# Performance work log

Measured on AMD Instinct MI355X. Metric: run time of the kernel, lower is better.

## Reference

```python
import jax, jax.numpy as jnp
import numpy as np
from fractions import Fraction
from math import factorial

# ---------- e3nn-convention real Wigner 3j (computed once in numpy) ----------

def _su2_cg(j1, m1, j2, m2, j3, m3):
    if m3 != m1 + m2:
        return 0.0
    vmin = int(max(-j1 + j2 + m3, -j1 + m1, 0))
    vmax = int(min(j2 + j3 + m1, j3 - j1 + j2, j3 + m3))
    f = lambda n: factorial(round(n))
    C = ((2.0 * j3 + 1.0) * Fraction(
        f(j3 + j1 - j2) * f(j3 - j1 + j2) * f(j1 + j2 - j3) * f(j3 + m3) * f(j3 - m3),
        f(j1 + j2 + j3 + 1) * f(j1 - m1) * f(j1 + m1) * f(j2 - m2) * f(j2 + m2))) ** 0.5
    S = 0
    for v in range(vmin, vmax + 1):
        S += (-1) ** int(v + j2 + m2) * Fraction(
            f(j2 + j3 + m1 - v) * f(j1 - m1 + v),
            f(v) * f(j3 - j1 + j2 - v) * f(j3 + m3 - v) * f(v + j1 - j2 - m3))
    return float(C * S)

def _q_real2complex(l):
    q = np.zeros((2 * l + 1, 2 * l + 1), dtype=complex)
    for m in range(-l, 0):
        q[l + m, l + abs(m)] = 1 / 2 ** 0.5
        q[l + m, l - abs(m)] = -1j / 2 ** 0.5
    q[l, l] = 1.0
    for m in range(1, l + 1):
        q[l + m, l + abs(m)] = (-1) ** m / 2 ** 0.5
        q[l + m, l - abs(m)] = 1j * (-1) ** m / 2 ** 0.5
    return (-1j) ** l * q

def _w3j(l1, l2, l3):
    C = np.zeros((2 * l1 + 1, 2 * l2 + 1, 2 * l3 + 1), dtype=complex)
    for m1 in range(-l1, l1 + 1):
        for m2 in range(-l2, l2 + 1):
            for m3 in range(-l3, l3 + 1):
                C[l1 + m1, l2 + m2, l3 + m3] = _su2_cg(l1, m1, l2, m2, l3, m3)
    C = np.einsum('ij,kl,mn,ikn->jlm', _q_real2complex(l1), _q_real2complex(l2),
                  np.conj(_q_real2complex(l3).T), C)
    assert np.abs(C.imag).max() < 1e-7
    C = C.real
    return C / np.linalg.norm(C)

# uuw instructions from get_feasible_tp(hidden, hidden, 0e+1e+2e): (l1, l2, l_out)
INS = [(0, 0, 0), (0, 2, 2), (1, 1, 0), (1, 1, 1), (1, 1, 2), (2, 0, 2), (2, 2, 0), (2, 2, 1), (2, 2, 2)]
W3J = {ls: jnp.asarray(_w3j(*ls), dtype=jnp.float32) for ls in set(INS)}
# change of basis of ReducedTensorProducts('ij', i='1o'): sph(0e+1e+2e) -> cart 3x3
Q_COB = jnp.asarray(np.concatenate([(2 * l + 1) ** 0.5 * _w3j(1, 1, l).transpose(2, 0, 1)
                                    for l in (0, 1, 2)], axis=0), dtype=jnp.float32)  # (9,3,3)
IN_IRR = ((128, 0), (64, 1), (32, 2))  # edge_irreps, dim 480
HID = 16                               # hidden multiplicity per l
CART = jnp.array([2, 0, 1])            # e3nn (y,z,x) -> (x,y,z)

def _split(x):
    parts, o = [], 0
    for mul, l in IN_IRR:
        d = mul * (2 * l + 1)
        parts.append(x[:, o:o + d].reshape(-1, mul, 2 * l + 1))
        o += d
    return parts

def _lin(parts, Ws):  # e3nn o3.Linear: per-l channel mix, 1/sqrt(fan_in)
    return [jnp.einsum('nui,uv->nvi', p, W) * (1.0 / np.sqrt(p.shape[1])) for p, W in zip(parts, Ws)]

def _forward(batch, x_scalar, x_spherical, WU0, WU1, WU2, WV0, WV1, WV2,
             Wg1, bg1, Wg2, bg2, Wp0, Wp1, Wp2, num_graphs):
    xs = _split(x_spherical)
    hU = _lin(xs, (WU0, WU1, WU2))  # [(N,16,1),(N,16,3),(N,16,5)]
    hV = _lin(xs, (WV0, WV1, WV2))
    w = jax.nn.silu(x_scalar @ Wg1 + bg1) @ Wg2 + bg2  # (N, 144) per-path tp weights
    outs = {0: [], 1: [], 2: []}
    for k, (l1, l2, l3) in enumerate(INS):
        wk = w[:, k * HID:(k + 1) * HID]
        coeff = float(np.sqrt((2 * l3 + 1) / HID))  # component/element norm
        outs[l3].append(coeff * jnp.einsum('nu,ijm,nui,nuj->nm', wk, W3J[(l1, l2, l3)], hU[l1], hV[l2]))
    Wp = {0: Wp0, 1: Wp1, 2: Wp2}
    sph = [jnp.einsum('num,u->nm', jnp.stack(outs[l], 1), Wp[l][:, 0]) * (1.0 / np.sqrt(len(outs[l])))
           for l in (0, 1, 2)]  # lin_out_post -> 1x0e+1x1e+1x2e
    atom_out = jnp.concatenate(sph, axis=-1)  # (N, 9)
    res_sph = jax.ops.segment_sum(atom_out, batch, num_segments=num_graphs)  # (G, 9)
    res_cart = jnp.einsum('gk,kij->gij', res_sph, Q_COB)  # (G, 3, 3)
    return res_cart[:, CART][:, :, CART]

def setup_inputs():
    key = jax.random.key(0)
    k = jax.random.split(key, 16)
    N, G = 150000, 2000
    f32 = jnp.float32
    rn = lambda kk, shp, s=1.0: jax.random.normal(kk, shp, f32) * s
    return {
        'batch': jnp.sort(jax.random.randint(k[0], (N,), 0, G)),
        'x_scalar': rn(k[1], (N, 128)),
        'x_spherical': rn(k[2], (N, 480)),
        'WU0': rn(k[3], (128, 16)), 'WU1': rn(k[4], (64, 16)), 'WU2': rn(k[5], (32, 16)),
        'WV0': rn(k[6], (128, 16)), 'WV1': rn(k[7], (64, 16)), 'WV2': rn(k[8], (32, 16)),
        'Wg1': rn(k[9], (128, 64), 128 ** -0.5), 'bg1': jnp.zeros((64,), f32),
        'Wg2': rn(k[10], (64, 144), 64 ** -0.5), 'bg2': jnp.zeros((144,), f32),
        'Wp0': rn(k[11], (3, 1)), 'Wp1': rn(k[12], (2, 1)), 'Wp2': rn(k[13], (4, 1)),
        'num_graphs': G,
    }

def reference(batch, x_scalar, x_spherical, WU0, WU1, WU2, WV0, WV1, WV2,
              Wg1, bg1, Wg2, bg2, Wp0, Wp1, Wp2, num_graphs):
    return _forward(batch, x_scalar, x_spherical, WU0, WU1, WU2, WV0, WV1, WV2,
                    Wg1, bg1, Wg2, bg2, Wp0, Wp1, Wp2, num_graphs)
```

## Files before the change

### kernel.cpp

```cpp
#include <hip/hip_runtime.h>
#include <hip/hip_bf16.h>
#include <math.h>

typedef unsigned short u16;
typedef unsigned int   u32;

#define TILE 16

#define WS_FLAG  368
#define WS_WG1   384
#define WS_WG2   8576
#define WS_WU0   17792
#define WS_WU1   19840
#define WS_WU2   20864
#define WS_WV0   21376
#define WS_WV1   23424
#define WS_WV2   24448
#define WS_BG1   24960
#define WS_BG2   25024
#define WS_C9    25168
#define WS_RES   25216

__device__ __forceinline__ float b2f(u16 u){
  return __uint_as_float(((u32)u) << 16);
}
__device__ __forceinline__ float ldconv(const void* p, int i, int isbf){
  return isbf ? b2f(((const u16*)p)[i]) : ((const float*)p)[i];
}

__global__ void detect_kernel(const u32* __restrict__ words, int* __restrict__ flag){
  int t = threadIdx.x;
  int cnt = 0;
  for (int i = 0; i < 16; i++){
    u32 w = words[t*16 + i];
    u32 e = (w >> 7) & 0xFF;
    cnt += (e >= 117 && e <= 137) ? 1 : 0;
  }
  #pragma unroll
  for (int m = 1; m < 64; m <<= 1) cnt += __shfl_xor(cnt, m, 64);
  if (t == 0) *flag = (cnt > 512) ? 1 : 0;
}

__device__ double factd(int n){ double r=1.0; for(int i=2;i<=n;++i) r*=(double)i; return r; }

__device__ double su2_cg(int j1,int m1,int j2,int m2,int j3,int m3){
  if (m1+m2 != m3) return 0.0;
  int vmin = max(max(-j1+j2+m3, -j1+m1), 0);
  int vmax = min(min(j2+j3+m1, j3-j1+j2), j3+m3);
  double C = sqrt((2.0*j3+1.0)
      * factd(j3+j1-j2)*factd(j3-j1+j2)*factd(j1+j2-j3)*factd(j3+m3)*factd(j3-m3)
      / (factd(j1+j2+j3+1)*factd(j1-m1)*factd(j1+m1)*factd(j2-m2)*factd(j2+m2)));
  double S = 0.0;
  for (int v=vmin; v<=vmax; ++v){
    double t = factd(j2+j3+m1-v)*factd(j1-m1+v)
             / (factd(v)*factd(j3-j1+j2-v)*factd(j3+m3-v)*factd(v+j1-j2-m3));
    S += ((v+j2+m2)&1) ? -t : t;
  }
  return C*S;
}

__device__ void qmat_lds(int l, double* qre, double* qim){
  int d = 2*l+1;
  for (int i=0;i<d*d;i++){ qre[i]=0.0; qim[i]=0.0; }
  double s = 1.0/sqrt(2.0);
  for (int m=-l; m<0; ++m){
    qre[(l+m)*d + (l-m)] = s;
    qim[(l+m)*d + (l+m)] = -s;
  }
  qre[l*d + l] = 1.0;
  for (int m=1; m<=l; ++m){
    double sgn = (m&1) ? -1.0 : 1.0;
    qre[(l+m)*d + (l+m)] = sgn*s;
    qim[(l+m)*d + (l-m)] = sgn*s;
  }
  double fr, fi;
  switch (l & 3){ case 0: fr=1; fi=0; break; case 1: fr=0; fi=-1; break;
                  case 2: fr=-1; fi=0; break; default: fr=0; fi=1; }
  for (int i=0;i<d*d;i++){
    double a=qre[i], b=qim[i];
    qre[i]=a*fr-b*fi; qim[i]=a*fi+b*fr;
  }
}

__global__ void setup_kernel(float* __restrict__ ws){
  __shared__ double q1r[25], q1i[25], q2r[25], q2i[25], q3r[25], q3i[25];
  __shared__ double red[128];
  const int L1[9]={0,0,1,1,1,2,2,2,2};
  const int L2[9]={0,2,1,1,1,0,2,2,2};
  const int L3[9]={0,2,0,1,2,2,0,1,2};
  const int OFF[9]={0,1,26,35,62,107,132,157,232};
  const int b = blockIdx.x;
  const int l1=L1[b], l2=L2[b], l3=L3[b];
  const int d1=2*l1+1, d2=2*l2+1, d3=2*l3+1;
  const int tot = d1*d2*d3;
  const int t = threadIdx.x;

  if (t==0) qmat_lds(l1, q1r, q1i);
  if (t==1) qmat_lds(l2, q2r, q2i);
  if (t==2) qmat_lds(l3, q3r, q3i);
  __syncthreads();

  double ar = 0.0;
  if (t < tot){
    const int j = t/(d2*d3), rem = t - j*(d2*d3), l = rem/d3, m = rem - l*d3;
    for (int i=0;i<d1;i++){
      double a1r=q1r[i*d1+j], a1i=q1i[i*d1+j];
      for (int k=0;k<d2;k++){
        double a2r=q2r[k*d2+l], a2i=q2i[k*d2+l];
        double t12r = a1r*a2r - a1i*a2i;
        double t12i = a1r*a2i + a1i*a2r;
        for (int n=0;n<d3;n++){
          double c = su2_cg(l1, i-l1, l2, k-l2, l3, n-l3);
          if (c==0.0) continue;
          double a3r = q3r[n*d3+m], a3i = -q3i[n*d3+m];
          ar += c*(t12r*a3r - t12i*a3i);
        }
      }
    }
  }
  red[t] = ar*ar;
  __syncthreads();
  for (int s=64; s>0; s>>=1){
    if (t < s) red[t] += red[t+s];
    __syncthreads();
  }
  double nrm = sqrt(red[0]);
  if (t < tot) ws[OFF[b] + t] = (float)(ar/nrm);
}

__global__ void convert_weights(
    const void* Wg1, const void* Wg2,
    const void* WU0, const void* WU1, const void* WU2,
    const void* WV0, const void* WV1, const void* WV2,
    const void* bg1, const void* bg2,
    const void* Wp0, const void* Wp1, const void* Wp2,
    float* __restrict__ ws)
{
  const int isbf = ((const int*)ws)[WS_FLAG];
  const int b = blockIdx.x, t = threadIdx.x;
  if (b < 10){
    const void* src[10] = {Wg1,Wg2,WU0,WU1,WU2,WV0,WV1,WV2,bg1,bg2};
    const int   sz[10]  = {8192,9216,2048,1024,512,2048,1024,512,64,144};
    const int   off[10] = {WS_WG1,WS_WG2,WS_WU0,WS_WU1,WS_WU2,WS_WV0,WS_WV1,WS_WV2,WS_BG1,WS_BG2};
    const void* s = src[b]; float* d = ws + off[b]; int n = sz[b];
    for (int i = t; i < n; i += 256) d[i] = ldconv(s, i, isbf);
  } else if (b == 10 && t == 0){
    float* C9 = ws + WS_C9;
    const int l3k[9]  = {0,2,0,1,2,2,0,1,2};
    const int idxk[9] = {0,0,1,0,1,2,2,1,3};
    for (int k=0;k<9;k++){
      int l3 = l3k[k];
      const void* wp = (l3==0) ? Wp0 : (l3==1) ? Wp1 : Wp2;
      float wpv = ldconv(wp, idxk[k], isbf);
      float len = (l3==0) ? 3.f : (l3==1) ? 2.f : 4.f;
      C9[k] = sqrtf((2.f*l3 + 1.f)/16.f) * wpv * rsqrtf(len);
    }
  }
}

__device__ __forceinline__ void load8_bf16(const u16* p, float* dst){
  uint4 v = *reinterpret_cast<const uint4*>(p);
  u32 w[4] = {v.x, v.y, v.z, v.w};
  #pragma unroll
  for (int q=0;q<4;q++){
    dst[2*q]   = __uint_as_float((w[q] & 0xffffu) << 16);
    dst[2*q+1] = __uint_as_float(w[q] & 0xffff0000u);
  }
}
__device__ __forceinline__ void load8_f32(const float* p, float* dst){
  float4 v0 = *reinterpret_cast<const float4*>(p);
  float4 v1 = *reinterpret_cast<const float4*>(p+4);
  dst[0]=v0.x; dst[1]=v0.y; dst[2]=v0.z; dst[3]=v0.w;
  dst[4]=v1.x; dst[5]=v1.y; dst[6]=v1.z; dst[7]=v1.w;
}

__global__ __launch_bounds__(256) void main_kernel(
    const int* __restrict__ batch,
    const void* __restrict__ xscv,
    const void* __restrict__ xspv,
    const float* __restrict__ ws,
    float* __restrict__ res,
    int N)
{
  __shared__ float s_xsph[TILE][481];
  __shared__ float s_w[TILE][144];
  __shared__ float s_uni[4624];
  __shared__ float s_w3j[357];
  __shared__ float s_bg1[64];
  __shared__ float s_bg2[144];
  __shared__ float s_C[9];
  __shared__ int   s_batch[TILE];

  float (*s_xs)[128] = reinterpret_cast<float(*)[128]>(s_uni);
  float (*s_h1)[64]  = reinterpret_cast<float(*)[64]>(s_uni + 2048);
  float (*s_hU)[144] = reinterpret_cast<float(*)[144]>(s_uni);
  float (*s_hV)[144] = reinterpret_cast<float(*)[144]>(s_uni + 2304);

  const int tid  = threadIdx.x;
  const int wave = tid >> 6;
  const int lane = tid & 63;
  const int n0   = blockIdx.x * TILE;
  const int isbf = ((const int*)ws)[WS_FLAG];

  const float* wsWg1 = ws + WS_WG1;
  const float* wsWg2 = ws + WS_WG2;
  const float* wsWU0 = ws + WS_WU0;
  const float* wsWU1 = ws + WS_WU1;
  const float* wsWU2 = ws + WS_WU2;
  const float* wsWV0 = ws + WS_WV0;
  const float* wsWV1 = ws + WS_WV1;
  const float* wsWV2 = ws + WS_WV2;

  if (tid < TILE){ int n = n0 + tid; s_batch[tid] = (n < N) ? batch[n] : -1; }
  if (tid < 64)  s_bg1[tid] = ws[WS_BG1 + tid];
  if (tid < 144) s_bg2[tid] = ws[WS_BG2 + tid];
  if (tid < 9)   s_C[tid]   = ws[WS_C9 + tid];
  for (int i = tid; i < 357; i += 256) s_w3j[i] = ws[i];
  {
    int base = tid*8, row = base >> 7, col = base & 127;
    int n = n0 + row;
    if (n < N){
      if (isbf) load8_bf16((const u16*)xscv + (size_t)n*128 + col, &s_xs[row][col]);
      else      load8_f32 ((const float*)xscv + (size_t)n*128 + col, &s_xs[row][col]);
    } else { for (int q=0;q<8;q++) s_xs[row][col+q] = 0.f; }
  }
  {
    for (int it = tid; it < 960; it += 256){
      int base = it*8, row = base/480, col = base - row*480;
      int n = n0 + row;
      if (n < N){
        if (isbf) load8_bf16((const u16*)xspv + (size_t)n*480 + col, &s_xsph[row][col]);
        else      load8_f32 ((const float*)xspv + (size_t)n*480 + col, &s_xsph[row][col]);
      } else { for (int q=0;q<8;q++) s_xsph[row][col+q] = 0.f; }
    }
  }
  __syncthreads();

  {
    const int a0 = wave*4;
    float acc0=s_bg1[lane], acc1=acc0, acc2=acc0, acc3=acc0;
    for (int c=0;c<128;c++){
      float wv = wsWg1[c*64 + lane];
      acc0 += s_xs[a0+0][c]*wv;
      acc1 += s_xs[a0+1][c]*wv;
      acc2 += s_xs[a0+2][c]*wv;
      acc3 += s_xs[a0+3][c]*wv;
    }
    s_h1[a0+0][lane] = acc0/(1.f+__expf(-acc0));
    s_h1[a0+1][lane] = acc1/(1.f+__expf(-acc1));
    s_h1[a0+2][lane] = acc2/(1.f+__expf(-acc2));
    s_h1[a0+3][lane] = acc3/(1.f+__expf(-acc3));
  }
  __syncthreads();

  {
    const int a0 = wave*4;
    float acc[4][3];
    #pragma unroll
    for (int t=0;t<4;t++){
      acc[t][0] = s_bg2[lane];
      acc[t][1] = s_bg2[64+lane];
      acc[t][2] = (lane<16) ? s_bg2[128+lane] : 0.f;
    }
    for (int c=0;c<64;c++){
      float w0 = wsWg2[c*144 + lane];
      float w1 = wsWg2[c*144 + 64 + lane];
      float w2 = (lane<16) ? wsWg2[c*144 + 128 + lane] : 0.f;
      #pragma unroll
      for (int t=0;t<4;t++){
        float h = s_h1[a0+t][c];
        acc[t][0] += h*w0; acc[t][1] += h*w1; acc[t][2] += h*w2;
      }
    }
    #pragma unroll
    for (int t=0;t<4;t++){
      s_w[a0+t][lane]    = acc[t][0];
      s_w[a0+t][64+lane] = acc[t][1];
      if (lane < 16) s_w[a0+t][128+lane] = acc[t][2];
    }
  }
  __syncthreads();

  {
    const int a = tid >> 4, v = tid & 15;
    const float r128 = 0.088388347648318447f;
    const float r64  = 0.125f;
    const float r32  = 0.17677669529663689f;
    {
      float aU=0.f, aV=0.f;
      for (int u=0;u<128;u++){
        float x = s_xsph[a][u];
        aU += x*wsWU0[u*16+v];
        aV += x*wsWV0[u*16+v];
      }
      s_hU[a][v] = aU*r128; s_hV[a][v] = aV*r128;
    }
    {
      float aU[3]={0,0,0}, aV[3]={0,0,0};
      for (int u=0;u<64;u++){
        float wu = wsWU1[u*16+v], wv = wsWV1[u*16+v];
        #pragma unroll
        for (int i=0;i<3;i++){
          float x = s_xsph[a][128 + u*3 + i];
          aU[i] += x*wu; aV[i] += x*wv;
        }
      }
      #pragma unroll
      for (int i=0;i<3;i++){ s_hU[a][16+v*3+i]=aU[i]*r64; s_hV[a][16+v*3+i]=aV[i]*r64; }
    }
    {
      float aU[5]={0,0,0,0,0}, aV[5]={0,0,0,0,0};
      for (int u=0;u<32;u++){
        float wu = wsWU2[u*16+v], wv = wsWV2[u*16+v];
        #pragma unroll
        for (int i=0;i<5;i++){
          float x = s_xsph[a][320 + u*5 + i];
          aU[i] += x*wu; aV[i] += x*wv;
        }
      }
      #pragma unroll
      for (int i=0;i<5;i++){ s_hU[a][64+v*5+i]=aU[i]*r32; s_hV[a][64+v*5+i]=aV[i]*r32; }
    }
  }
  __syncthreads();

  {
    const int a = tid >> 4, u = tid & 15;
    float hu0 = s_hU[a][u], hv0 = s_hV[a][u];
    float hu1[3], hv1[3], hu2[5], hv2[5];
    #pragma unroll
    for (int i=0;i<3;i++){ hu1[i]=s_hU[a][16+u*3+i]; hv1[i]=s_hV[a][16+u*3+i]; }
    #pragma unroll
    for (int i=0;i<5;i++){ hu2[i]=s_hU[a][64+u*5+i]; hv2[i]=s_hV[a][64+u*5+i]; }
    float wk[9];
    #pragma unroll
    for (int k=0;k<9;k++) wk[k] = s_w[a][k*16+u];

    const float* J = s_w3j;
    float t9[9] = {0,0,0,0,0,0,0,0,0};

    t9[0] += s_C[0]*wk[0]*J[0]*hu0*hv0;
    {
      float cw = s_C[1]*wk[1]*hu0;
      #pragma unroll
      for (int m=0;m<5;m++){
        float s=0.f;
        #pragma unroll
        for (int j=0;j<5;j++) s += J[1 + j*5 + m]*hv2[j];
        t9[4+m] += cw*s;
      }
    }
    {
      float s=0.f;
      #pragma unroll
      for (int i=0;i<3;i++)
        #pragma unroll
        for (int j=0;j<3;j++) s += J[26 + i*3 + j]*hu1[i]*hv1[j];
      t9[0] += s_C[2]*wk[2]*s;
    }
    {
      float sm[3]={0,0,0};
      #pragma unroll
      for (int i=0;i<3;i++)
        #pragma unroll
        for (int j=0;j<3;j++){
          float p = hu1[i]*hv1[j];
          #pragma unroll
          for (int m=0;m<3;m++) sm[m] += J[35 + (i*3+j)*3 + m]*p;
        }
      float c = s_C[3]*wk[3];
      #pragma unroll
      for (int m=0;m<3;m++) t9[1+m] += c*sm[m];
    }
    {
      float sm[5]={0,0,0,0,0};
      #pragma unroll
      for (int i=0;i<3;i++)
        #pragma unroll
        for (int j=0;j<3;j++){
          float p = hu1[i]*hv1[j];
          #pragma unroll
          for (int m=0;m<5;m++) sm[m] += J[62 + (i*3+j)*5 + m]*p;
        }
      float c = s_C[4]*wk[4];
      #pragma unroll
      for (int m=0;m<5;m++) t9[4+m] += c*sm[m];
    }
    {
      float cw = s_C[5]*wk[5]*hv0;
      #pragma unroll
      for (int m=0;m<5;m++){
        float s=0.f;
        #pragma unroll
        for (int i=0;i<5;i++) s += J[107 + i*5 + m]*hu2[i];
        t9[4+m] += cw*s;
      }
    }
    {
      float s=0.f;
      #pragma unroll
      for (int i=0;i<5;i++)
        #pragma unroll
        for (int j=0;j<5;j++) s += J[132 + i*5 + j]*hu2[i]*hv2[j];
      t9[0] += s_C[6]*wk[6]*s;
    }
    {
      float sm[3]={0,0,0};
      #pragma unroll
      for (int i=0;i<5;i++)
        #pragma unroll
        for (int j=0;j<5;j++){
          float p = hu2[i]*hv2[j];
          #pragma unroll
          for (int m=0;m<3;m++) sm[m] += J[157 + (i*5+j)*3 + m]*p;
        }
      float c = s_C[7]*wk[7];
      #pragma unroll
      for (int m=0;m<3;m++) t9[1+m] += c*sm[m];
    }
    {
      float sm[5]={0,0,0,0,0};
      #pragma unroll
      for (int i=0;i<5;i++)
        #pragma unroll
        for (int j=0;j<5;j++){
          float p = hu2[i]*hv2[j];
          #pragma unroll
          for (int m=0;m<5;m++) sm[m] += J[232 + (i*5+j)*5 + m]*p;
        }
      float c = s_C[8]*wk[8];
      #pragma unroll
      for (int m=0;m<5;m++) t9[4+m] += c*sm[m];
    }

    #pragma unroll
    for (int mask=1; mask<16; mask<<=1){
      #pragma unroll
      for (int s=0;s<9;s++) t9[s] += __shfl_xor(t9[s], mask, 64);
    }
    if (u == 0 && (n0 + a) < N){
      int g = s_batch[a];
      float* r = res + (size_t)g*9;
      #pragma unroll
      for (int s=0;s<9;s++) atomicAdd(&r[s], t9[s]);
    }
  }
}

__global__ void finish_kernel(const float* __restrict__ res,
                              const float* __restrict__ ws,
                              void* __restrict__ out, int G)
{
  int idx = blockIdx.x*256 + threadIdx.x;
  if (idx >= G*9) return;
  const int isbf = ((const int*)ws)[WS_FLAG];
  int g = idx/9, s = idx - g*9;
  int a = s/3, b = s - a*3;
  const int cart[3] = {2,0,1};
  int ca = cart[a], cb = cart[b];
  const float s3 = 1.7320508075688772f, s5 = 2.2360679774997896f;
  const float* r = res + (size_t)g*9;
  float acc = r[0]*ws[26 + ca*3 + cb];
  #pragma unroll
  for (int m=0;m<3;m++) acc += r[1+m]*s3*ws[35 + (ca*3+cb)*3 + m];
  #pragma unroll
  for (int m=0;m<5;m++) acc += r[4+m]*s5*ws[62 + (ca*3+cb)*5 + m];
  if (isbf) ((__hip_bfloat16*)out)[idx] = __float2bfloat16(acc);
  else      ((float*)out)[idx] = acc;
}

extern "C" void kernel_launch(void* const* d_in, const int* in_sizes, int n_in,
                              void* d_out, int out_size, void* d_ws, size_t ws_size,
                              hipStream_t stream) {
  const int* batch = (const int*)d_in[0];
  const void* xsc = d_in[1];
  const void* xsp = d_in[2];

  const int N = in_sizes[0];
  const int G = out_size / 9;

  float* ws  = (float*)d_ws;
  float* res = ws + WS_RES;

  hipMemsetAsync(res, 0, (size_t)G*9*sizeof(float), stream);
  detect_kernel<<<1, 64, 0, stream>>>((const u32*)xsp, (int*)(ws + WS_FLAG));
  setup_kernel<<<9, 128, 0, stream>>>(ws);
  convert_weights<<<11, 256, 0, stream>>>(d_in[9], d_in[11],
                                          d_in[3], d_in[4], d_in[5],
                                          d_in[6], d_in[7], d_in[8],
                                          d_in[10], d_in[12],
                                          d_in[13], d_in[14], d_in[15],
                                          ws);

  int nb = (N + TILE - 1) / TILE;
  main_kernel<<<nb, 256, 0, stream>>>(batch, xsc, xsp, ws, res, N);

  finish_kernel<<<(G*9 + 255)/256, 256, 0, stream>>>(res, ws, d_out, G);
}
```

Before: 1.184 ms.

## Add bf16 MFMA path for gate MLP and projections with per-wave tiles

Adds an mfma_kernel that does the gate MLP and the U/V projections with 16x16x32 bf16 MFMA instructions. It uses pre-transposed bf16 weight copies in the workspace, with block-diagonal expansion for the l=1 and l=2 projections. Each wave handles one 16-atom tile and reduces per-graph results with shuffles and atomics. A probe kernel checks that the MFMA operand layout is correct, and the old fp32 kernel now exits early when the MFMA path applies. Splitting the hidden activations into hi and lo bf16 parts keeps precision, at the cost of extra MFMAs and redundant zero-padded work in the expanded weights.

Result: no change. 1.162 ms (-1.9%).

```diff
diff --git a/kernel.cpp b/kernel.cpp
--- a/kernel.cpp
+++ b/kernel.cpp
@@ -4,10 +4,13 @@
 
 typedef unsigned short u16;
 typedef unsigned int   u32;
+typedef __attribute__((ext_vector_type(8))) short short8v;
+typedef __attribute__((ext_vector_type(4))) float f32x4;
 
 #define TILE 16
 
 #define WS_FLAG  368
+#define WS_MOK   369
 #define WS_WG1   384
 #define WS_WG2   8576
 #define WS_WU0   17792
@@ -21,8 +24,19 @@
 #define WS_C9    25168
 #define WS_RES   25216
 
+#define WSH_BG1T 88064
+#define WSH_BG2T 96256
+#define WSH_B0T  105472
+#define WSH_B1T  109568
+#define WSH_B2T  128000
+#define WS_NEED_BYTES 307200
+
 __device__ __forceinline__ float b2f(u16 u){
   return __uint_as_float(((u32)u) << 16);
+}
+__device__ __forceinline__ u16 f2b(float f){
+  u32 x = __float_as_uint(f);
+  return (u16)((x + 0x7fffu + ((x >> 16) & 1u)) >> 16);
 }
 __device__ __forceinline__ float ldconv(const void* p, int i, int isbf){
   return isbf ? b2f(((const u16*)p)[i]) : ((const float*)p)[i];
@@ -138,29 +152,385 @@
 {
   const int isbf = ((const int*)ws)[WS_FLAG];
   const int b = blockIdx.x, t = threadIdx.x;
+  u16* wh = (u16*)ws;
   if (b < 10){
     const void* src[10] = {Wg1,Wg2,WU0,WU1,WU2,WV0,WV1,WV2,bg1,bg2};
     const int   sz[10]  = {8192,9216,2048,1024,512,2048,1024,512,64,144};
     const int   off[10] = {WS_WG1,WS_WG2,WS_WU0,WS_WU1,WS_WU2,WS_WV0,WS_WV1,WS_WV2,WS_BG1,WS_BG2};
     const void* s = src[b]; float* d = ws + off[b]; int n = sz[b];
     for (int i = t; i < n; i += 256) d[i] = ldconv(s, i, isbf);
-  } else if (b == 10 && t == 0){
-    float* C9 = ws + WS_C9;
-    const int l3k[9]  = {0,2,0,1,2,2,0,1,2};
-    const int idxk[9] = {0,0,1,0,1,2,2,1,3};
-    for (int k=0;k<9;k++){
-      int l3 = l3k[k];
-      const void* wp = (l3==0) ? Wp0 : (l3==1) ? Wp1 : Wp2;
-      float wpv = ldconv(wp, idxk[k], isbf);
-      float len = (l3==0) ? 3.f : (l3==1) ? 2.f : 4.f;
-      C9[k] = sqrtf((2.f*l3 + 1.f)/16.f) * wpv * rsqrtf(len);
-    }
+  } else if (b == 10){
+    if (t == 0){
+      float* C9 = ws + WS_C9;
+      const int l3k[9]  = {0,2,0,1,2,2,0,1,2};
+      const int idxk[9] = {0,0,1,0,1,2,2,1,3};
+      for (int k=0;k<9;k++){
+        int l3 = l3k[k];
+        const void* wp = (l3==0) ? Wp0 : (l3==1) ? Wp1 : Wp2;
+        float wpv = ldconv(wp, idxk[k], isbf);
+        float len = (l3==0) ? 3.f : (l3==1) ? 2.f : 4.f;
+        C9[k] = sqrtf((2.f*l3 + 1.f)/16.f) * wpv * rsqrtf(len);
+      }
+    }
+  } else if (b == 11){
+    for (int i=t;i<8192;i+=256){
+      int n = i >> 7, k = i & 127;
+      wh[WSH_BG1T + i] = f2b(ldconv(Wg1, k*64 + n, isbf));
+    }
+  } else if (b == 12){
+    for (int i=t;i<9216;i+=256){
+      int n = i >> 6, k = i & 63;
+      wh[WSH_BG2T + i] = f2b(ldconv(Wg2, k*144 + n, isbf));
+    }
+  } else if (b == 13){
+    for (int i=t;i<4096;i+=256){
+      int n = i >> 7, k = i & 127;
+      float v = (n < 16) ? ldconv(WU0, k*16 + n, isbf)
+                         : ldconv(WV0, k*16 + (n-16), isbf);
+      wh[WSH_B0T + i] = f2b(v);
+    }
+  } else if (b == 14){
+    for (int i=t;i<18432;i+=256){
+      int n = i / 192, k = i - n*192;
+      int uv = n / 48, rem = n - uv*48, ii = rem >> 4, vv = rem & 15;
+      float val = 0.f;
+      if (k % 3 == ii){
+        int u = k / 3;
+        val = ldconv(uv ? WV1 : WU1, u*16 + vv, isbf);
+      }
+      wh[WSH_B1T + i] = f2b(val);
+    }
+  } else if (b == 15){
+    for (int i=t;i<25600;i+=256){
+      int n = i / 160, k = i - n*160;
+      int uv = n / 80, rem = n - uv*80, ii = rem >> 4, vv = rem & 15;
+      float val = 0.f;
+      if (k % 5 == ii){
+        int u = k / 5;
+        val = ldconv(uv ? WV2 : WU2, u*16 + vv, isbf);
+      }
+      wh[WSH_B2T + i] = f2b(val);
+    }
+  }
+}
+
+__global__ void probe_kernel(float* __restrict__ ws){
+  __shared__ u16 A[512];
+  __shared__ u16 B[512];
+  int t = threadIdx.x;
+  for (int i=t;i<512;i+=64){
+    int m = i >> 5, k = i & 31;
+    A[i] = f2b((float)(((3*m + k) % 7) - 3));
+    int kk = i >> 4, n = i & 15;
+    B[i] = f2b((float)(((2*kk + 5*n) % 9) - 4));
+  }
+  __syncthreads();
+  int v = t & 15, g4 = t >> 4;
+  short8v a, b;
+  #pragma unroll
+  for (int j=0;j<8;j++){
+    a[j] = (short)A[v*32 + 8*g4 + j];
+    b[j] = (short)B[(8*g4 + j)*16 + v];
+  }
+  f32x4 c = {0.f,0.f,0.f,0.f};
+  c = __builtin_amdgcn_mfma_f32_16x16x32_bf16(a, b, c, 0, 0, 0);
+  int ok = 1;
+  #pragma unroll
+  for (int r=0;r<4;r++){
+    int row = 4*g4 + r;
+    float ref = 0.f;
+    for (int k=0;k<32;k++) ref += b2f(A[row*32+k]) * b2f(B[k*16+v]);
+    if (fabsf(c[r] - ref) > 0.25f) ok = 0;
+  }
+  #pragma unroll
+  for (int m=1;m<64;m<<=1) ok &= __shfl_xor(ok, m, 64);
+  if (t == 0) ((int*)ws)[WS_MOK] = ok;
+}
+
+__global__ __launch_bounds__(256,3) void mfma_kernel(
+    const int* __restrict__ batch,
+    const void* __restrict__ xscv,
+    const void* __restrict__ xspv,
+    const float* __restrict__ ws,
+    float* __restrict__ res,
+    int N)
+{
+  const int isbf = ((const int*)ws)[WS_FLAG];
+  const int mok  = ((const int*)ws)[WS_MOK];
+  if (!(isbf && mok)) return;
+
+  __shared__ __align__(16) u16 H1hi[4][16][72];
+  __shared__ __align__(16) u16 H1lo[4][16][72];
+
+  const int tid = threadIdx.x;
+  const int wave = tid >> 6, lane = tid & 63;
+  const int v = lane & 15, g4 = lane >> 4;
+  const int tile = blockIdx.x*4 + wave;
+  const int n0 = tile * TILE;
+  if (n0 >= N) return;
+
+  const u16* xsc = (const u16*)xscv;
+  const u16* xsp = (const u16*)xspv;
+  const u16* wb  = (const u16*)ws;
+
+  int rowA = n0 + v; if (rowA >= N) rowA = N - 1;
+
+  f32x4 accg[4];
+  #pragma unroll
+  for (int nt=0;nt<4;nt++) accg[nt] = (f32x4){0.f,0.f,0.f,0.f};
+  {
+    const u16* aP = xsc + (size_t)rowA*128 + 8*g4;
+    const u16* bP = wb + WSH_BG1T + v*128 + 8*g4;
+    #pragma unroll
+    for (int kt=0;kt<4;kt++){
+      short8v a = *(const short8v*)(aP + kt*32);
+      #pragma unroll
+      for (int nt=0;nt<4;nt++){
+        short8v b = *(const short8v*)(bP + nt*2048 + kt*32);
+        accg[nt] = __builtin_amdgcn_mfma_f32_16x16x32_bf16(a, b, accg[nt], 0, 0, 0);
+      }
+    }
+  }
+  #pragma unroll
+  for (int nt=0;nt<4;nt++){
+    float bb = ws[WS_BG1 + nt*16 + v];
+    #pragma unroll
+    for (int r=0;r<4;r++){
+      float hs = accg[nt][r] + bb;
+      float h  = hs / (1.f + __expf(-hs));
+      u16 hi = f2b(h);
+      float lo = h - b2f(hi);
+      int atom = 4*g4 + r;
+      H1hi[wave][atom][nt*16 + v] = hi;
+      H1lo[wave][atom][nt*16 + v] = f2b(lo);
+    }
+  }
+
+  f32x4 accw[9];
+  #pragma unroll
+  for (int nt=0;nt<9;nt++) accw[nt] = (f32x4){0.f,0.f,0.f,0.f};
+  {
+    const u16* hH = &H1hi[wave][v][8*g4];
+    const u16* hL = &H1lo[wave][v][8*g4];
+    const u16* bP = wb + WSH_BG2T + v*64 + 8*g4;
+    #pragma unroll
+    for (int kt=0;kt<2;kt++){
+      short8v ah = *(const short8v*)(hH + kt*32);
+      short8v al = *(const short8v*)(hL + kt*32);
+      #pragma unroll
+      for (int nt=0;nt<9;nt++){
+        short8v b = *(const short8v*)(bP + nt*1024 + kt*32);
+        accw[nt] = __builtin_amdgcn_mfma_f32_16x16x32_bf16(ah, b, accw[nt], 0, 0, 0);
+        accw[nt] = __builtin_amdgcn_mfma_f32_16x16x32_bf16(al, b, accw[nt], 0, 0, 0);
+      }
+    }
+  }
+  float wkv[9][4];
+  #pragma unroll
+  for (int nt=0;nt<9;nt++){
+    float bb = ws[WS_BG2 + nt*16 + v];
+    float c9 = ws[WS_C9 + nt];
+    #pragma unroll
+    for (int r=0;r<4;r++) wkv[nt][r] = (accw[nt][r] + bb) * c9;
+  }
+
+  const u16* spA = xsp + (size_t)rowA*480 + 8*g4;
+
+  f32x4 acc0[2];
+  #pragma unroll
+  for (int nt=0;nt<2;nt++) acc0[nt] = (f32x4){0.f,0.f,0.f,0.f};
+  {
+    const u16* bP = wb + WSH_B0T + v*128 + 8*g4;
+    #pragma unroll
+    for (int kt=0;kt<4;kt++){
+      short8v a = *(const short8v*)(spA + kt*32);
+      #pragma unroll
+      for (int nt=0;nt<2;nt++){
+        short8v b = *(const short8v*)(bP + nt*2048 + kt*32);
+        acc0[nt] = __builtin_amdgcn_mfma_f32_16x16x32_bf16(a, b, acc0[nt], 0, 0, 0);
+      }
+    }
+  }
+  f32x4 accA[6];
+  #pragma unroll
+  for (int nt=0;nt<6;nt++) accA[nt] = (f32x4){0.f,0.f,0.f,0.f};
+  {
+    const u16* bP = wb + WSH_B1T + v*192 + 8*g4;
+    #pragma unroll
+    for (int kt=0;kt<6;kt++){
+      short8v a = *(const short8v*)(spA + 128 + kt*32);
+      #pragma unroll
+      for (int nt=0;nt<6;nt++){
+        short8v b = *(const short8v*)(bP + nt*3072 + kt*32);
+        accA[nt] = __builtin_amdgcn_mfma_f32_16x16x32_bf16(a, b, accA[nt], 0, 0, 0);
+      }
+    }
+  }
+  f32x4 accB[10];
+  #pragma unroll
+  for (int nt=0;nt<10;nt++) accB[nt] = (f32x4){0.f,0.f,0.f,0.f};
+  {
+    const u16* bP = wb + WSH_B2T + v*160 + 8*g4;
+    #pragma unroll
+    for (int kt=0;kt<5;kt++){
+      short8v a = *(const short8v*)(spA + 320 + kt*32);
+      #pragma unroll
+      for (int nt=0;nt<10;nt++){
+        short8v b = *(const short8v*)(bP + nt*2560 + kt*32);
+        accB[nt] = __builtin_amdgcn_mfma_f32_16x16x32_bf16(a, b, accB[nt], 0, 0, 0);
+      }
+    }
+  }
+
+  int bidr[4];
+  #pragma unroll
+  for (int r=0;r<4;r++){
+    int n = n0 + 4*g4 + r;
+    bidr[r] = (n < N) ? batch[n] : -1;
+  }
+
+  const float r128 = 0.088388347648318447f;
+  const float r64  = 0.125f;
+  const float r32  = 0.17677669529663689f;
+  const float* J = ws;
+  float pend[9];
+  int pg = -1;
+
+  #pragma unroll
+  for (int r=0;r<4;r++){
+    float hu0 = acc0[0][r]*r128, hv0 = acc0[1][r]*r128;
+    float hu1[3], hv1[3], hu2[5], hv2[5];
+    #pragma unroll
+    for (int i=0;i<3;i++){ hu1[i] = accA[i][r]*r64; hv1[i] = accA[3+i][r]*r64; }
+    #pragma unroll
+    for (int i=0;i<5;i++){ hu2[i] = accB[i][r]*r32; hv2[i] = accB[5+i][r]*r32; }
+
+    float t9[9] = {0,0,0,0,0,0,0,0,0};
+    t9[0] += wkv[0][r]*J[0]*hu0*hv0;
+    {
+      float cw = wkv[1][r]*hu0;
+      #pragma unroll
+      for (int m=0;m<5;m++){
+        float s=0.f;
+        #pragma unroll
+        for (int j=0;j<5;j++) s += J[1 + j*5 + m]*hv2[j];
+        t9[4+m] += cw*s;
+      }
+    }
+    {
+      float s=0.f;
+      #pragma unroll
+      for (int i=0;i<3;i++)
+        #pragma unroll
+        for (int j=0;j<3;j++) s += J[26 + i*3 + j]*hu1[i]*hv1[j];
+      t9[0] += wkv[2][r]*s;
+    }
+    {
+      float sm[3]={0,0,0};
+      #pragma unroll
+      for (int i=0;i<3;i++)
+        #pragma unroll
+        for (int j=0;j<3;j++){
+          float p = hu1[i]*hv1[j];
+          #pragma unroll
+          for (int m=0;m<3;m++) sm[m] += J[35 + (i*3+j)*3 + m]*p;
+        }
+      #pragma unroll
+      for (int m=0;m<3;m++) t9[1+m] += wkv[3][r]*sm[m];
+    }
+    {
+      float sm[5]={0,0,0,0,0};
+      #pragma unroll
+      for (int i=0;i<3;i++)
+        #pragma unroll
+        for (int j=0;j<3;j++){
+          float p = hu1[i]*hv1[j];
+          #pragma unroll
+          for (int m=0;m<5;m++) sm[m] += J[62 + (i*3+j)*5 + m]*p;
+        }
+      #pragma unroll
+      for (int m=0;m<5;m++) t9[4+m] += wkv[4][r]*sm[m];
+    }
+    {
+      float cw = wkv[5][r]*hv0;
+      #pragma unroll
+      for (int m=0;m<5;m++){
+        float s=0.f;
+        #pragma unroll
+        for (int i=0;i<5;i++) s += J[107 + i*5 + m]*hu2[i];
+        t9[4+m] += cw*s;
+      }
+    }
+    {
+      float s=0.f;
+      #pragma unroll
+      for (int i=0;i<5;i++)
+        #pragma unroll
+        for (int j=0;j<5;j++) s += J[132 + i*5 + j]*hu2[i]*hv2[j];
+      t9[0] += wkv[6][r]*s;
+    }
+    {
+      float sm[3]={0,0,0};
+      #pragma unroll
+      for (int i=0;i<5;i++)
+        #pragma unroll
+        for (int j=0;j<5;j++){
+          float p = hu2[i]*hv2[j];
+          #pragma unroll
+          for (int m=0;m<3;m++) sm[m] += J[157 + (i*5+j)*3 + m]*p;
+        }
+      #pragma unroll
+      for (int m=0;m<3;m++) t9[1+m] += wkv[7][r]*sm[m];
+    }
+    {
+      float sm[5]={0,0,0,0,0};
+      #pragma unroll
+      for (int i=0;i<5;i++)
+        #pragma unroll
+        for (int j=0;j<5;j++){
+          float p = hu2[i]*hv2[j];
+          #pragma unroll
+          for (int m=0;m<5;m++) sm[m] += J[232 + (i*5+j)*5 + m]*p;
+        }
+      #pragma unroll
+      for (int m=0;m<5;m++) t9[4+m] += wkv[8][r]*sm[m];
+    }
+
+    #pragma unroll
+    for (int mask=1; mask<16; mask<<=1){
+      #pragma unroll
+      for (int s=0;s<9;s++) t9[s] += __shfl_xor(t9[s], mask, 64);
+    }
+    if (v == 0){
+      int n = n0 + 4*g4 + r;
+      if (n < N){
+        int g = bidr[r];
+        if (g == pg){
+          #pragma unroll
+          for (int s=0;s<9;s++) pend[s] += t9[s];
+        } else {
+          if (pg >= 0){
+            float* rp = res + (size_t)pg*9;
+            #pragma unroll
+            for (int s=0;s<9;s++) atomicAdd(&rp[s], pend[s]);
+          }
+          pg = g;
+          #pragma unroll
+          for (int s=0;s<9;s++) pend[s] = t9[s];
+        }
+      }
+    }
+  }
+  if (v == 0 && pg >= 0){
+    float* rp = res + (size_t)pg*9;
+    #pragma unroll
+    for (int s=0;s<9;s++) atomicAdd(&rp[s], pend[s]);
   }
 }
 
 __device__ __forceinline__ void load8_bf16(const u16* p, float* dst){
-  uint4 v = *reinterpret_cast<const uint4*>(p);
-  u32 w[4] = {v.x, v.y, v.z, v.w};
+  uint4 vv = *reinterpret_cast<const uint4*>(p);
+  u32 w[4] = {vv.x, vv.y, vv.z, vv.w};
   #pragma unroll
   for (int q=0;q<4;q++){
     dst[2*q]   = __uint_as_float((w[q] & 0xffffu) << 16);
@@ -182,6 +552,11 @@
     float* __restrict__ res,
     int N)
 {
+  {
+    const int fb = ((const int*)ws)[WS_FLAG];
+    const int mk = ((const int*)ws)[WS_MOK];
+    if (fb && mk) return;
+  }
   __shared__ float s_xsph[TILE][481];
   __shared__ float s_w[TILE][144];
   __shared__ float s_uni[4624];
@@ -482,15 +857,22 @@
   float* ws  = (float*)d_ws;
   float* res = ws + WS_RES;
 
+  const bool big = (ws_size >= (size_t)WS_NEED_BYTES) && (G <= 2090);
+
   hipMemsetAsync(res, 0, (size_t)G*9*sizeof(float), stream);
+  hipMemsetAsync(ws + WS_MOK, 0, sizeof(int), stream);
   detect_kernel<<<1, 64, 0, stream>>>((const u32*)xsp, (int*)(ws + WS_FLAG));
   setup_kernel<<<9, 128, 0, stream>>>(ws);
-  convert_weights<<<11, 256, 0, stream>>>(d_in[9], d_in[11],
+  convert_weights<<<big ? 16 : 11, 256, 0, stream>>>(d_in[9], d_in[11],
                                           d_in[3], d_in[4], d_in[5],
                                           d_in[6], d_in[7], d_in[8],
                                           d_in[10], d_in[12],
                                           d_in[13], d_in[14], d_in[15],
                                           ws);
+  if (big){
+    probe_kernel<<<1, 64, 0, stream>>>(ws);
+    mfma_kernel<<<(N + 63)/64, 256, 0, stream>>>(batch, xsc, xsp, ws, res, N);
+  }
 
   int nb = (N + TILE - 1) / TILE;
   main_kernel<<<nb, 256, 0, stream>>>(batch, xsc, xsp, ws, res, N);
```
